# Optimization experiments

Measured on AMD Instinct MI355X. Metric: run time of the kernel, lower is better.

## Reference

```python
import jax, jax.numpy as jnp
import numpy as np

B, T, J = 8, 1024, 25
D_MODEL, D_STATE, D_CONV, EXPAND = 256, 16, 4, 2
D_INNER = EXPAND * D_MODEL            # 512
DT_RANK = (D_MODEL + 15) // 16        # 16
N_CLASSES = 60


def layernorm(x, g, b, eps=1e-5):
    mu = x.mean(-1, keepdims=True)
    var = ((x - mu) ** 2).mean(-1, keepdims=True)
    return (x - mu) * jax.lax.rsqrt(var + eps) * g + b


def selective_scan(u, delta, A, Bm, Cm, D):
    # u, delta: [b,l,d]; A: [d,n]; Bm, Cm: [b,l,n]; D: [d]
    dA = jnp.exp(delta[..., None] * A)                              # [b,l,d,n]
    dBu = delta[..., None] * Bm[:, :, None, :] * u[..., None]        # [b,l,d,n]

    def step(h, inp):
        dA_t, dBu_t, C_t = inp
        h = dA_t * h + dBu_t                                         # [b,d,n]
        y = jnp.einsum('bdn,bn->bd', h, C_t)
        return h, y

    h0 = jnp.zeros((u.shape[0], u.shape[2], A.shape[1]), u.dtype)
    _, ys = jax.lax.scan(step, h0, (jnp.moveaxis(dA, 1, 0),
                                    jnp.moveaxis(dBu, 1, 0),
                                    jnp.moveaxis(Cm, 1, 0)))
    return jnp.moveaxis(ys, 0, 1) + u * D                            # [b,l,d]


def setup_inputs() -> dict:
    key = jax.random.key(0)
    ks = jax.random.split(key, 12)
    rn = lambda k, s, sc=0.02: jax.random.normal(k, s, jnp.float32) * sc
    A_log = jnp.log(jnp.tile(jnp.arange(1, D_STATE + 1, dtype=jnp.float32), (D_INNER, 1)))
    return {
        'x': jax.random.normal(ks[0], (B, T, J, 3), jnp.float32),
        'embed_w': rn(ks[1], (D_MODEL, J * 9)), 'embed_b': jnp.zeros((D_MODEL,), jnp.float32),
        'pre_g': jnp.ones((D_MODEL,), jnp.float32), 'pre_b': jnp.zeros((D_MODEL,), jnp.float32),
        'in_proj_w': rn(ks[2], (2 * D_INNER, D_MODEL)),
        'conv_w': rn(ks[3], (D_INNER, 1, D_CONV)), 'conv_b': jnp.zeros((D_INNER,), jnp.float32),
        'x_proj_w': rn(ks[4], (DT_RANK + 2 * D_STATE, D_INNER)),
        'dt_proj_w': rn(ks[5], (D_INNER, DT_RANK)), 'dt_proj_b': rn(ks[6], (D_INNER,), 0.1),
        'A_log': A_log, 'D': jnp.ones((D_INNER,), jnp.float32),
        'out_proj_w': rn(ks[7], (D_MODEL, D_INNER)),
        'post_g': jnp.ones((D_MODEL,), jnp.float32), 'post_b': jnp.zeros((D_MODEL,), jnp.float32),
        'fine_w': rn(ks[8], (N_CLASSES, D_MODEL)), 'fine_b': jnp.zeros((N_CLASSES,), jnp.float32),
    }


def reference(x, embed_w, embed_b, pre_g, pre_b, in_proj_w, conv_w, conv_b,
              x_proj_w, dt_proj_w, dt_proj_b, A_log, D, out_proj_w,
              post_g, post_b, fine_w, fine_b):
    b, t = x.shape[0], x.shape[1]
    # --- SkeletonNormalizer: root-center (scale_joints=None) ---
    pos = x[..., :3] - x[:, :, 0:1, :3]                              # [B,T,J,3]
    # --- MotionFeatureBuilder: pos / vel / acc ---
    vel = jnp.concatenate([jnp.zeros_like(pos[:, :1]), pos[:, 1:] - pos[:, :-1]], axis=1)
    acc = jnp.concatenate([jnp.zeros_like(vel[:, :1]), vel[:, 1:] - vel[:, :-1]], axis=1)
    feat = jnp.concatenate([pos, vel, acc], axis=-1).reshape(b, t, -1)  # [B,T,J*9]
    # --- embed ---
    feat = feat @ embed_w.T + embed_b                                # [B,T,D_MODEL]
    # --- Mamba block on pre-norm, residual add ---
    hn = layernorm(feat, pre_g, pre_b)
    xz = hn @ in_proj_w.T                                            # [B,T,2*D_INNER]
    xm, res = jnp.split(xz, 2, axis=-1)
    # depthwise causal conv1d over time
    xm = jax.lax.conv_general_dilated(
        jnp.swapaxes(xm, 1, 2), conv_w, (1,), [(D_CONV - 1, 0)],
        dimension_numbers=('NCH', 'OIH', 'NCH'), feature_group_count=D_INNER)
    xm = jnp.swapaxes(xm + conv_b[None, :, None], 1, 2)              # [B,T,D_INNER]
    xm = jax.nn.silu(xm)
    dbl = xm @ x_proj_w.T                                            # [B,T,DT_RANK+2*D_STATE]
    dt = dbl[..., :DT_RANK]
    Bm = dbl[..., DT_RANK:DT_RANK + D_STATE]
    Cm = dbl[..., DT_RANK + D_STATE:]
    delta = jax.nn.softplus(dt @ dt_proj_w.T + dt_proj_b)            # [B,T,D_INNER]
    A = -jnp.exp(A_log)                                              # [D_INNER,D_STATE]
    y = selective_scan(xm, delta, A, Bm, Cm, D)
    y = y * jax.nn.silu(res)
    y = y @ out_proj_w.T                                             # [B,T,D_MODEL]
    feat = feat + y
    # --- post norm, mean pool, classify ---
    feat = layernorm(feat, post_g, post_b)
    pooled = feat.mean(axis=1)                                       # [B,D_MODEL]
    return pooled @ fine_w.T + fine_b                                # [B,N_CLASSES]
```

## Files before the change

kernel.cpp:

```cpp
#include <hip/hip_runtime.h>
#include <hip/hip_bf16.h>
#include <math.h>

#define Bb 8
#define Tt 1024
#define Jj 25
#define D_MODEL 256
#define D_STATE 16
#define D_CONV 4
#define D_INNER 512
#define DT_RANK 16
#define N_CLASSES 60
#define Mrows (Bb*Tt)
#define NC 64
#define CL 16

typedef unsigned short u16;
using bf16x8 = __attribute__((ext_vector_type(8))) __bf16;
using f32x4  = __attribute__((ext_vector_type(4))) float;

__device__ inline u16 f2bf(float x) {
    unsigned u = __float_as_uint(x);
    unsigned r = (u + 0x7fffu + ((u >> 16) & 1u)) >> 16;
    return (u16)r;
}
__device__ inline float bf2f(u16 h) { return __uint_as_float((unsigned)h << 16); }
__device__ inline void split2(float x, u16& h, u16& l) {
    h = f2bf(x);
    l = f2bf(x - bf2f(h));
}
__device__ inline float softplus_fast(float s) {
    return fmaxf(s, 0.f) + __logf(1.f + __expf(-fabsf(s)));
}
__device__ inline f32x4 mfma3(bf16x8 ah, bf16x8 al, bf16x8 bh, bf16x8 bl, f32x4 c) {
    c = __builtin_amdgcn_mfma_f32_16x16x32_bf16(al, bh, c, 0, 0, 0);
    c = __builtin_amdgcn_mfma_f32_16x16x32_bf16(ah, bl, c, 0, 0, 0);
    c = __builtin_amdgcn_mfma_f32_16x16x32_bf16(ah, bh, c, 0, 0, 0);
    return c;
}

__global__ __launch_bounds__(256) void prep_kernel(
    const float* __restrict__ x, u16* __restrict__ fh, u16* __restrict__ fl,
    const float* __restrict__ ew, const float* __restrict__ iw,
    const float* __restrict__ xw, const float* __restrict__ ow,
    u16* __restrict__ ebh, u16* __restrict__ ebl,
    u16* __restrict__ iph, u16* __restrict__ ipl,
    u16* __restrict__ xph, u16* __restrict__ xpl,
    u16* __restrict__ oph, u16* __restrict__ opl) {
    int blk = blockIdx.x;
    if (blk < Mrows) {
        int r = blk;
        int c = threadIdx.x;
        float v = 0.f;
        if (c < 225) {
            int t = r & (Tt - 1);
            int j = c / 9;
            int cc = c - j * 9;
            int comp = cc % 3;
            int kind = cc / 3;
            auto POS = [&](int dt) -> float {
                const float* p = x + (long)(r - dt) * Jj * 3;
                return p[j * 3 + comp] - p[comp];
            };
            if (kind == 0) v = POS(0);
            else if (kind == 1) v = (t >= 1) ? (POS(0) - POS(1)) : 0.f;
            else {
                if (t >= 2)      v = POS(0) - 2.f * POS(1) + POS(2);
                else if (t == 1) v = POS(0) - POS(1);
                else             v = 0.f;
            }
        }
        u16 h, l;
        split2(v, h, l);
        fh[(long)r * 256 + c] = h;
        fl[(long)r * 256 + c] = l;
    } else {
        int i = (blk - Mrows) * 256 + threadIdx.x;
        const float* src; u16 *dh, *dl; int K, kshift, idx;
        if (i < 65536)       { src = ew; dh = ebh; dl = ebl; K = 225; kshift = 8; idx = i; }
        else if (i < 327680) { src = iw; dh = iph; dl = ipl; K = 256; kshift = 8; idx = i - 65536; }
        else if (i < 352256) { src = xw; dh = xph; dl = xpl; K = 512; kshift = 9; idx = i - 327680; }
        else                 { src = ow; dh = oph; dl = opl; K = 512; kshift = 9; idx = i - 352256; }
        int n = idx >> kshift;
        int k = idx & ((1 << kshift) - 1);
        float v = (k < K) ? src[(long)n * K + k] : 0.f;
        u16 h, l;
        split2(v, h, l);
        dh[idx] = h;
        dl[idx] = l;
    }
}

template<int BM, int BN, int EPI>
__global__ __launch_bounds__(256) void gemm_mfma(
    const u16* __restrict__ Ahi, const u16* __restrict__ Alo, int lda,
    const u16* __restrict__ Whi, const u16* __restrict__ Wlo, int ldw,
    const float* __restrict__ bias, const float* __restrict__ resid, int ldr,
    float* __restrict__ C, int ldc, int M, int N, int K)
{
    constexpr int TM = BM / 32;
    constexpr int TN = BN / 32;
    constexpr int SA = 40;
    __shared__ u16 AsH[BM * SA], AsL[BM * SA];
    __shared__ u16 WsH[BN * SA], WsL[BN * SA];
    int tid = threadIdx.x;
    int m0 = blockIdx.y * BM;
    int n0 = blockIdx.x * BN;
    int lane = tid & 63;
    int wave = tid >> 6;
    int wm = wave >> 1, wn = wave & 1;
    int fr = lane & 15, quad = lane >> 4;
    f32x4 acc[TM][TN] = {};

    for (int k0 = 0; k0 < K; k0 += 32) {
        for (int s = tid; s < BM * 4; s += 256) {
            int row = s >> 2, seg = s & 3;
            long off = (long)(m0 + row) * lda + k0 + seg * 8;
            *(uint4*)&AsH[row * SA + seg * 8] = *(const uint4*)(Ahi + off);
            *(uint4*)&AsL[row * SA + seg * 8] = *(const uint4*)(Alo + off);
        }
        for (int s = tid; s < BN * 4; s += 256) {
            int row = s >> 2, seg = s & 3;
            long off = (long)(n0 + row) * ldw + k0 + seg * 8;
            *(uint4*)&WsH[row * SA + seg * 8] = *(const uint4*)(Whi + off);
            *(uint4*)&WsL[row * SA + seg * 8] = *(const uint4*)(Wlo + off);
        }
        __syncthreads();
        bf16x8 aH[TM], aL[TM], bH[TN], bL[TN];
#pragma unroll
        for (int im = 0; im < TM; im++) {
            int r = wm * (BM / 2) + im * 16 + fr;
            aH[im] = *(const bf16x8*)&AsH[r * SA + quad * 8];
            aL[im] = *(const bf16x8*)&AsL[r * SA + quad * 8];
        }
#pragma unroll
        for (int in = 0; in < TN; in++) {
            int r = wn * (BN / 2) + in * 16 + fr;
            bH[in] = *(const bf16x8*)&WsH[r * SA + quad * 8];
            bL[in] = *(const bf16x8*)&WsL[r * SA + quad * 8];
        }
#pragma unroll
        for (int im = 0; im < TM; im++)
#pragma unroll
            for (int in = 0; in < TN; in++)
                acc[im][in] = mfma3(aH[im], aL[im], bH[in], bL[in], acc[im][in]);
        __syncthreads();
    }
#pragma unroll
    for (int im = 0; im < TM; im++) {
#pragma unroll
        for (int in = 0; in < TN; in++) {
#pragma unroll
            for (int reg = 0; reg < 4; reg++) {
                int gm = m0 + wm * (BM / 2) + im * 16 + quad * 4 + reg;
                int gn = n0 + wn * (BN / 2) + in * 16 + fr;
                float v = acc[im][in][reg];
                if (EPI == 1) v += bias[gn];
                if (EPI == 3) v += resid[(long)gm * ldr + gn];
                C[(long)gm * ldc + gn] = v;
            }
        }
    }
}

__global__ __launch_bounds__(256) void ln_kernel(const float* __restrict__ x,
                                                 const float* __restrict__ g,
                                                 const float* __restrict__ b,
                                                 u16* outh, u16* outl) {
    __shared__ float red[256];
    long r = blockIdx.x;
    int d = threadIdx.x;
    float v = x[r * 256 + d];
    red[d] = v;
    __syncthreads();
    for (int s = 128; s > 0; s >>= 1) {
        if (d < s) red[d] += red[d + s];
        __syncthreads();
    }
    float mu = red[0] * (1.f / 256.f);
    __syncthreads();
    float dv = v - mu;
    red[d] = dv * dv;
    __syncthreads();
    for (int s = 128; s > 0; s >>= 1) {
        if (d < s) red[d] += red[d + s];
        __syncthreads();
    }
    float var = red[0] * (1.f / 256.f);
    float o = dv * rsqrtf(var + 1e-5f) * g[d] + b[d];
    u16 h, l;
    split2(o, h, l);
    outh[r * 256 + d] = h;
    outl[r * 256 + d] = l;
}

__global__ __launch_bounds__(256) void ln_pool_kernel(const float* __restrict__ x,
                                                      const float* __restrict__ g,
                                                      const float* __restrict__ b,
                                                      float* __restrict__ bp) {
    __shared__ float red[256];
    long r = blockIdx.x;
    int d = threadIdx.x;
    float v = x[r * 256 + d];
    red[d] = v;
    __syncthreads();
    for (int s = 128; s > 0; s >>= 1) {
        if (d < s) red[d] += red[d + s];
        __syncthreads();
    }
    float mu = red[0] * (1.f / 256.f);
    __syncthreads();
    float dv = v - mu;
    red[d] = dv * dv;
    __syncthreads();
    for (int s = 128; s > 0; s >>= 1) {
        if (d < s) red[d] += red[d + s];
        __syncthreads();
    }
    float var = red[0] * (1.f / 256.f);
    float o = dv * rsqrtf(var + 1e-5f) * g[d] + b[d];
    atomicAdd(&bp[(r >> 6) * 256 + d], o);
}

__global__ __launch_bounds__(256) void conv_xproj_kernel(
    const float* __restrict__ xz,
    const float* __restrict__ cw, const float* __restrict__ cb,
    const u16* __restrict__ Whi, const u16* __restrict__ Wlo,
    u16* __restrict__ xmh, u16* __restrict__ xml,
    float* __restrict__ dbl)
{
    constexpr int SA = 40;
    __shared__ u16 AsH[16 * SA], AsL[16 * SA];
    __shared__ u16 WsH[64 * SA], WsL[64 * SA];
    int tid = threadIdx.x;
    int m0 = blockIdx.x * 16;
    int lane = tid & 63, wave = tid >> 6;
    int fr = lane & 15, quad = lane >> 4;
    f32x4 acc = {};

    if (tid < 64) {
        int wr = 48 + (tid >> 2), seg = tid & 3;
        *(uint4*)&WsH[wr * SA + seg * 8] = make_uint4(0, 0, 0, 0);
        *(uint4*)&WsL[wr * SA + seg * 8] = make_uint4(0, 0, 0, 0);
    }

    int row = tid >> 4;
    int cg  = tid & 15;
    long gr = m0 + row;
    int t = gr & (Tt - 1);
    const float* xzr = xz + gr * 1024;

    for (int k0 = 0; k0 < 512; k0 += 32) {
        int c0 = k0 + cg * 2;
        float2 x0 = *(const float2*)(xzr + c0);
        float2 x1 = (t >= 1) ? *(const float2*)(xzr - 1024 + c0) : make_float2(0, 0);
        float2 x2 = (t >= 2) ? *(const float2*)(xzr - 2048 + c0) : make_float2(0, 0);
        float2 x3 = (t >= 3) ? *(const float2*)(xzr - 3072 + c0) : make_float2(0, 0);
        u16 hh0, ll0, hh1, ll1;
        {
            float4 w = *(const float4*)(cw + (c0 + 0) * 4);
            float a = cb[c0 + 0] + w.w * x0.x + w.z * x1.x + w.y * x2.x + w.x * x3.x;
            float s = a / (1.f + __expf(-a));
            split2(s, hh0, ll0);
            w = *(const float4*)(cw + (c0 + 1) * 4);
            a = cb[c0 + 1] + w.w * x0.y + w.z * x1.y + w.y * x2.y + w.x * x3.y;
            s = a / (1.f + __expf(-a));
            split2(s, hh1, ll1);
        }
        unsigned ph = hh0 | ((unsigned)hh1 << 16);
        unsigned pl = ll0 | ((unsigned)ll1 << 16);
        *(unsigned*)(xmh + gr * 512 + c0) = ph;
        *(unsigned*)(xml + gr * 512 + c0) = pl;
        *(unsigned*)&AsH[row * SA + cg * 2] = ph;
        *(unsigned*)&AsL[row * SA + cg * 2] = pl;
        if (tid < 192) {
            int wr = tid >> 2, seg = tid & 3;
            long off = (long)wr * 512 + k0 + seg * 8;
            *(uint4*)&WsH[wr * SA + seg * 8] = *(const uint4*)(Whi + off);
            *(uint4*)&WsL[wr * SA + seg * 8] = *(const uint4*)(Wlo + off);
        }
        __syncthreads();
        bf16x8 aH = *(const bf16x8*)&AsH[fr * SA + quad * 8];
        bf16x8 aL = *(const bf16x8*)&AsL[fr * SA + quad * 8];
        int wrow = wave * 16 + fr;
        bf16x8 bH = *(const bf16x8*)&WsH[wrow * SA + quad * 8];
        bf16x8 bL = *(const bf16x8*)&WsL[wrow * SA + quad * 8];
        acc = mfma3(aH, aL, bH, bL, acc);
        __syncthreads();
    }
    int gn = wave * 16 + fr;
    if (gn < 48) {
#pragma unroll
        for (int reg = 0; reg < 4; reg++) {
            int gm = m0 + quad * 4 + reg;
            dbl[(long)gm * 48 + gn] = acc[reg];
        }
    }
}

__global__ __launch_bounds__(512) void scan_p1(const float* __restrict__ dbl,
                                               const float* __restrict__ dtw,
                                               const float* __restrict__ dtb,
                                               const u16* __restrict__ xmh,
                                               const u16* __restrict__ xml,
                                               const float* __restrict__ A_log,
                                               float* __restrict__ chunkS,
                                               float* __restrict__ sumdelta) {
    __shared__ float ds[CL * 48];
    int b = blockIdx.x, c = blockIdx.y, d = threadIdx.x;
    long r0 = (long)b * Tt + (long)c * CL;
    for (int i = d; i < CL * 48; i += 512) ds[i] = dbl[r0 * 48 + i];

    float Arow[16];
#pragma unroll
    for (int n = 0; n < 16; n++) Arow[n] = -expf(A_log[d * 16 + n]);
    float4 wd[4];
#pragma unroll
    for (int q = 0; q < 4; q++) wd[q] = *(const float4*)(dtw + d * 16 + q * 4);
    float bdt = dtb[d];
    float S[16];
#pragma unroll
    for (int n = 0; n < 16; n++) S[n] = 0.f;
    float sd = 0.f;
    __syncthreads();

    for (int t = 0; t < CL; t++) {
        const float* row = ds + t * 48;
        float4 t0 = *(const float4*)(row + 0);
        float4 t1 = *(const float4*)(row + 4);
        float4 t2 = *(const float4*)(row + 8);
        float4 t3 = *(const float4*)(row + 12);
        float s = bdt;
        s += t0.x * wd[0].x + t0.y * wd[0].y + t0.z * wd[0].z + t0.w * wd[0].w;
        s += t1.x * wd[1].x + t1.y * wd[1].y + t1.z * wd[1].z + t1.w * wd[1].w;
        s += t2.x * wd[2].x + t2.y * wd[2].y + t2.z * wd[2].z + t2.w * wd[2].w;
        s += t3.x * wd[3].x + t3.y * wd[3].y + t3.z * wd[3].z + t3.w * wd[3].w;
        float dl = softplus_fast(s);
        long r = r0 + t;
        float u = bf2f(xmh[r * 512 + d]) + bf2f(xml[r * 512 + d]);
        float du = dl * u;
        sd += dl;
        float Bn[16];
#pragma unroll
        for (int q = 0; q < 4; q++) {
            float4 bv = *(const float4*)(row + 16 + q * 4);
            Bn[q*4+0] = bv.x; Bn[q*4+1] = bv.y; Bn[q*4+2] = bv.z; Bn[q*4+3] = bv.w;
        }
#pragma unroll
        for (int n = 0; n < 16; n++) {
            float a = __expf(dl * Arow[n]);
            S[n] = a * S[n] + du * Bn[n];
        }
    }
    long base = ((long)(b * NC + c) * 16) * 512 + d;
#pragma unroll
    for (int n = 0; n < 16; n++) chunkS[base + (long)n * 512] = S[n];
    sumdelta[(long)(b * NC + c) * 512 + d] = sd;
}

__global__ __launch_bounds__(256) void scan_combine(float* chunkS,
                                                    const float* __restrict__ sumdelta,
                                                    const float* __restrict__ A_log) {
    int idx = blockIdx.x * 256 + threadIdx.x;
    int d = idx & 511;
    int n = (idx >> 9) & 15;
    int b = idx >> 13;
    float Aval = -expf(A_log[d * 16 + n]);
    float h = 0.f;
    for (int c = 0; c < NC; c++) {
        long si = ((long)(b * NC + c) * 16 + n) * 512 + d;
        float s = chunkS[si];
        float a = __expf(Aval * sumdelta[(long)(b * NC + c) * 512 + d]);
        chunkS[si] = h;
        h = a * h + s;
    }
}

__global__ __launch_bounds__(512) void scan_p2(const float* __restrict__ dbl,
                                               const float* __restrict__ dtw,
                                               const float* __restrict__ dtb,
                                               const u16* xmh, const u16* xml,
                                               const float* __restrict__ xz,
                                               const float* __restrict__ A_log,
                                               const float* __restrict__ Dv,
                                               const float* __restrict__ chunkH,
                                               u16* yh, u16* yl) {
    __shared__ float ds[CL * 48];
    int b = blockIdx.x, c = blockIdx.y, d = threadIdx.x;
    long r0 = (long)b * Tt + (long)c * CL;
    for (int i = d; i < CL * 48; i += 512) ds[i] = dbl[r0 * 48 + i];

    float Arow[16];
#pragma unroll
    for (int n = 0; n < 16; n++) Arow[n] = -expf(A_log[d * 16 + n]);
    float4 wd[4];
#pragma unroll
    for (int q = 0; q < 4; q++) wd[q] = *(const float4*)(dtw + d * 16 + q * 4);
    float bdt = dtb[d];
    float Dd = Dv[d];
    float h[16];
    long base = ((long)(b * NC + c) * 16) * 512 + d;
#pragma unroll
    for (int n = 0; n < 16; n++) h[n] = chunkH[base + (long)n * 512];
    __syncthreads();

    for (int t = 0; t < CL; t++) {
        const float* row = ds + t * 48;
        float4 t0 = *(const float4*)(row + 0);
        float4 t1 = *(const float4*)(row + 4);
        float4 t2 = *(const float4*)(row + 8);
        float4 t3 = *(const float4*)(row + 12);
        float s = bdt;
        s += t0.x * wd[0].x + t0.y * wd[0].y + t0.z * wd[0].z + t0.w * wd[0].w;
        s += t1.x * wd[1].x + t1.y * wd[1].y + t1.z * wd[1].z + t1.w * wd[1].w;
        s += t2.x * wd[2].x + t2.y * wd[2].y + t2.z * wd[2].z + t2.w * wd[2].w;
        s += t3.x * wd[3].x + t3.y * wd[3].y + t3.z * wd[3].z + t3.w * wd[3].w;
        float dl = softplus_fast(s);
        long r = r0 + t;
        float u = bf2f(xmh[r * 512 + d]) + bf2f(xml[r * 512 + d]);
        float res = xz[r * 1024 + 512 + d];
        float du = dl * u;
        float Bn[16], Cn[16];
#pragma unroll
        for (int q = 0; q < 4; q++) {
            float4 bv = *(const float4*)(row + 16 + q * 4);
            float4 cv = *(const float4*)(row + 32 + q * 4);
            Bn[q*4+0] = bv.x; Bn[q*4+1] = bv.y; Bn[q*4+2] = bv.z; Bn[q*4+3] = bv.w;
            Cn[q*4+0] = cv.x; Cn[q*4+1] = cv.y; Cn[q*4+2] = cv.z; Cn[q*4+3] = cv.w;
        }
        float ysum = 0.f;
#pragma unroll
        for (int n = 0; n < 16; n++) {
            float a = __expf(dl * Arow[n]);
            h[n] = a * h[n] + du * Bn[n];
            ysum += h[n] * Cn[n];
        }
        float yy = ysum + u * Dd;
        float sres = res / (1.f + __expf(-res));
        float outv = yy * sres;
        u16 hh, ll;
        split2(outv, hh, ll);
        yh[r * 512 + d] = hh;
        yl[r * 512 + d] = ll;
    }
}

__global__ __launch_bounds__(256) void head_kernel(const float* __restrict__ bp,
                                                   const float* __restrict__ fw,
                                                   const float* __restrict__ fb,
                                                   float* __restrict__ out) {
    __shared__ float pld[256];
    int b = blockIdx.x;
    int d = threadIdx.x;
    float s = 0.f;
#pragma unroll
    for (int i = 0; i < 16; i++)
        s += bp[(long)(b * 16 + i) * 256 + d];
    pld[d] = s;
    __syncthreads();
    if (d < N_CLASSES) {
        float acc = 0.f;
        for (int k = 0; k < 256; k++) acc += pld[k] * fw[d * 256 + k];
        out[b * N_CLASSES + d] = acc * (1.f / (float)Tt) + fb[d];
    }
}

extern "C" void kernel_launch(void* const* d_in, const int* in_sizes, int n_in,
                              void* d_out, int out_size, void* d_ws, size_t ws_size,
                              hipStream_t stream) {
    const float* x         = (const float*)d_in[0];
    const float* embed_w   = (const float*)d_in[1];
    const float* embed_b   = (const float*)d_in[2];
    const float* pre_g     = (const float*)d_in[3];
    const float* pre_b     = (const float*)d_in[4];
    const float* in_proj_w = (const float*)d_in[5];
    const float* conv_w    = (const float*)d_in[6];
    const float* conv_b    = (const float*)d_in[7];
    const float* x_proj_w  = (const float*)d_in[8];
    const float* dt_proj_w = (const float*)d_in[9];
    const float* dt_proj_b = (const float*)d_in[10];
    const float* A_log     = (const float*)d_in[11];
    const float* Dv        = (const float*)d_in[12];
    const float* out_proj_w= (const float*)d_in[13];
    const float* post_g    = (const float*)d_in[14];
    const float* post_b    = (const float*)d_in[15];
    const float* fine_w    = (const float*)d_in[16];
    const float* fine_b    = (const float*)d_in[17];
    float* out = (float*)d_out;
    char* base = (char*)d_ws;

    float* feat     = (float*)(base + 0);
    float* xz       = (float*)(base + 8388608);
    float* chunkS   = (float*)(base + 41943040);
    u16*   xmh      = (u16*)  (base + 58720256);
    u16*   xml      = (u16*)  (base + 67108864);
    u16*   fbh      = (u16*)  (base + 75497472);
    u16*   fbl      = (u16*)  (base + 79691776);
    float* dbl      = (float*)(base + 83886080);
    float* sumdelta = (float*)(base + 85458944);
    float* blockpart= (float*)(base + 86507520);
    u16*   ebh      = (u16*)  (base + 86638592);
    u16*   ebl      = ebh + 65536;
    u16*   iph      = ebl + 65536;
    u16*   ipl      = iph + 262144;
    u16*   xph      = ipl + 262144;
    u16*   xpl      = xph + 24576;
    u16*   oph      = xpl + 24576;
    u16*   opl      = oph + 131072;

    prep_kernel<<<dim3(Mrows + 1888), dim3(256), 0, stream>>>(
        x, fbh, fbl, embed_w, in_proj_w, x_proj_w, out_proj_w,
        ebh, ebl, iph, ipl, xph, xpl, oph, opl);

    gemm_mfma<64,64,1><<<dim3(4, 128), dim3(256), 0, stream>>>(
        fbh, fbl, 256, ebh, ebl, 256, embed_b, nullptr, 0, feat, 256, Mrows, 256, 256);

    ln_kernel<<<dim3(Mrows), dim3(256), 0, stream>>>(feat, pre_g, pre_b, fbh, fbl);

    gemm_mfma<128,64,0><<<dim3(16, 64), dim3(256), 0, stream>>>(
        fbh, fbl, 256, iph, ipl, 256, nullptr, nullptr, 0, xz, 1024, Mrows, 1024, 256);

    conv_xproj_kernel<<<dim3(Mrows / 16), dim3(256), 0, stream>>>(
        xz, conv_w, conv_b, xph, xpl, xmh, xml, dbl);

    scan_p1<<<dim3(Bb, NC), dim3(512), 0, stream>>>(
        dbl, dt_proj_w, dt_proj_b, xmh, xml, A_log, chunkS, sumdelta);
    scan_combine<<<dim3(256), dim3(256), 0, stream>>>(chunkS, sumdelta, A_log);
    scan_p2<<<dim3(Bb, NC), dim3(512), 0, stream>>>(
        dbl, dt_proj_w, dt_proj_b, xmh, xml, xz, A_log, Dv, chunkS, xmh, xml);

    gemm_mfma<64,64,3><<<dim3(4, 128), dim3(256), 0, stream>>>(
        xmh, xml, 512, oph, opl, 512, nullptr, feat, 256, feat, 256, Mrows, 256, 512);

    hipMemsetAsync(blockpart, 0, 128 * 256 * sizeof(float), stream);
    ln_pool_kernel<<<dim3(Mrows), dim3(256), 0, stream>>>(feat, post_g, post_b, blockpart);

    head_kernel<<<dim3(Bb), dim3(256), 0, stream>>>(blockpart, fine_w, fine_b, out);
}
```

Measured before the change: 260.9 us.

## Fuse chunked scan phases into one cooperative kernel with grid syncs

Merges scan_p1, scan_combine and scan_p2 into a single cooperative kernel separated by grid.sync. Each block keeps its chunk's dt-projection inputs, A row and u values in registers across phases, so the second pass no longer reloads xm or recomputes setup. The blockpart memset moves into extra blocks of the prep kernel, and the loops are reshaped to read B and C directly from float4. This trades two launches for grid-wide barriers, adds register pressure from uu[16], and leaves most blocks idle during the combine phase.

```diff
diff --git a/kernel.cpp b/kernel.cpp
--- a/kernel.cpp
+++ b/kernel.cpp
@@ -1,6 +1,9 @@
 #include <hip/hip_runtime.h>
 #include <hip/hip_bf16.h>
+#include <hip/hip_cooperative_groups.h>
 #include <math.h>
+
+namespace cg = cooperative_groups;
 
 #define Bb 8
 #define Tt 1024
@@ -46,7 +49,8 @@
     u16* __restrict__ ebh, u16* __restrict__ ebl,
     u16* __restrict__ iph, u16* __restrict__ ipl,
     u16* __restrict__ xph, u16* __restrict__ xpl,
-    u16* __restrict__ oph, u16* __restrict__ opl) {
+    u16* __restrict__ oph, u16* __restrict__ opl,
+    float* __restrict__ blockpart) {
     int blk = blockIdx.x;
     if (blk < Mrows) {
         int r = blk;
@@ -74,7 +78,7 @@
         split2(v, h, l);
         fh[(long)r * 256 + c] = h;
         fl[(long)r * 256 + c] = l;
-    } else {
+    } else if (blk < Mrows + 1888) {
         int i = (blk - Mrows) * 256 + threadIdx.x;
         const float* src; u16 *dh, *dl; int K, kshift, idx;
         if (i < 65536)       { src = ew; dh = ebh; dl = ebl; K = 225; kshift = 8; idx = i; }
@@ -88,6 +92,9 @@
         split2(v, h, l);
         dh[idx] = h;
         dl[idx] = l;
+    } else {
+        int i = (blk - Mrows - 1888) * 256 + threadIdx.x;
+        blockpart[i] = 0.f;
     }
 }
 
@@ -298,14 +305,16 @@
     }
 }
 
-__global__ __launch_bounds__(512) void scan_p1(const float* __restrict__ dbl,
-                                               const float* __restrict__ dtw,
-                                               const float* __restrict__ dtb,
-                                               const u16* __restrict__ xmh,
-                                               const u16* __restrict__ xml,
-                                               const float* __restrict__ A_log,
-                                               float* __restrict__ chunkS,
-                                               float* __restrict__ sumdelta) {
+__global__ __launch_bounds__(512, 4) void scan_fused(
+    const float* __restrict__ dbl,
+    const float* __restrict__ dtw, const float* __restrict__ dtb,
+    const u16* xmh, const u16* xml,
+    const float* __restrict__ xz,
+    const float* __restrict__ A_log, const float* __restrict__ Dv,
+    float* chunkS, float* sumdelta,
+    u16* yh, u16* yl)
+{
+    cg::grid_group grid = cg::this_grid();
     __shared__ float ds[CL * 48];
     int b = blockIdx.x, c = blockIdx.y, d = threadIdx.x;
     long r0 = (long)b * Tt + (long)c * CL;
@@ -318,6 +327,7 @@
 #pragma unroll
     for (int q = 0; q < 4; q++) wd[q] = *(const float4*)(dtw + d * 16 + q * 4);
     float bdt = dtb[d];
+    float uu[CL];
     float S[16];
 #pragma unroll
     for (int n = 0; n < 16; n++) S[n] = 0.f;
@@ -338,71 +348,50 @@
         float dl = softplus_fast(s);
         long r = r0 + t;
         float u = bf2f(xmh[r * 512 + d]) + bf2f(xml[r * 512 + d]);
+        uu[t] = u;
         float du = dl * u;
         sd += dl;
-        float Bn[16];
 #pragma unroll
         for (int q = 0; q < 4; q++) {
             float4 bv = *(const float4*)(row + 16 + q * 4);
-            Bn[q*4+0] = bv.x; Bn[q*4+1] = bv.y; Bn[q*4+2] = bv.z; Bn[q*4+3] = bv.w;
-        }
-#pragma unroll
-        for (int n = 0; n < 16; n++) {
-            float a = __expf(dl * Arow[n]);
-            S[n] = a * S[n] + du * Bn[n];
-        }
-    }
-    long base = ((long)(b * NC + c) * 16) * 512 + d;
-#pragma unroll
-    for (int n = 0; n < 16; n++) chunkS[base + (long)n * 512] = S[n];
+            float a0 = __expf(dl * Arow[q*4+0]); S[q*4+0] = a0 * S[q*4+0] + du * bv.x;
+            float a1 = __expf(dl * Arow[q*4+1]); S[q*4+1] = a1 * S[q*4+1] + du * bv.y;
+            float a2 = __expf(dl * Arow[q*4+2]); S[q*4+2] = a2 * S[q*4+2] + du * bv.z;
+            float a3 = __expf(dl * Arow[q*4+3]); S[q*4+3] = a3 * S[q*4+3] + du * bv.w;
+        }
+    }
+    long basei = ((long)(b * NC + c) * 16) * 512 + d;
+#pragma unroll
+    for (int n = 0; n < 16; n++) chunkS[basei + (long)n * 512] = S[n];
     sumdelta[(long)(b * NC + c) * 512 + d] = sd;
-}
-
-__global__ __launch_bounds__(256) void scan_combine(float* chunkS,
-                                                    const float* __restrict__ sumdelta,
-                                                    const float* __restrict__ A_log) {
-    int idx = blockIdx.x * 256 + threadIdx.x;
-    int d = idx & 511;
-    int n = (idx >> 9) & 15;
-    int b = idx >> 13;
-    float Aval = -expf(A_log[d * 16 + n]);
-    float h = 0.f;
-    for (int c = 0; c < NC; c++) {
-        long si = ((long)(b * NC + c) * 16 + n) * 512 + d;
-        float s = chunkS[si];
-        float a = __expf(Aval * sumdelta[(long)(b * NC + c) * 512 + d]);
-        chunkS[si] = h;
-        h = a * h + s;
-    }
-}
-
-__global__ __launch_bounds__(512) void scan_p2(const float* __restrict__ dbl,
-                                               const float* __restrict__ dtw,
-                                               const float* __restrict__ dtb,
-                                               const u16* xmh, const u16* xml,
-                                               const float* __restrict__ xz,
-                                               const float* __restrict__ A_log,
-                                               const float* __restrict__ Dv,
-                                               const float* __restrict__ chunkH,
-                                               u16* yh, u16* yl) {
-    __shared__ float ds[CL * 48];
-    int b = blockIdx.x, c = blockIdx.y, d = threadIdx.x;
-    long r0 = (long)b * Tt + (long)c * CL;
-    for (int i = d; i < CL * 48; i += 512) ds[i] = dbl[r0 * 48 + i];
-
-    float Arow[16];
-#pragma unroll
-    for (int n = 0; n < 16; n++) Arow[n] = -expf(A_log[d * 16 + n]);
-    float4 wd[4];
-#pragma unroll
-    for (int q = 0; q < 4; q++) wd[q] = *(const float4*)(dtw + d * 16 + q * 4);
-    float bdt = dtb[d];
+
+    __threadfence();
+    grid.sync();
+
+    int bid = blockIdx.y * 8 + blockIdx.x;
+    if (bid < 128) {
+        int idx = bid * 512 + d;
+        int dd = idx & 511;
+        int nn = (idx >> 9) & 15;
+        int bb = idx >> 13;
+        float Aval = -expf(A_log[dd * 16 + nn]);
+        float h = 0.f;
+        for (int cc = 0; cc < NC; cc++) {
+            long si = ((long)(bb * NC + cc) * 16 + nn) * 512 + dd;
+            float s = chunkS[si];
+            float a = __expf(Aval * sumdelta[(long)(bb * NC + cc) * 512 + dd]);
+            chunkS[si] = h;
+            h = a * h + s;
+        }
+    }
+
+    __threadfence();
+    grid.sync();
+
     float Dd = Dv[d];
     float h[16];
-    long base = ((long)(b * NC + c) * 16) * 512 + d;
-#pragma unroll
-    for (int n = 0; n < 16; n++) h[n] = chunkH[base + (long)n * 512];
-    __syncthreads();
+#pragma unroll
+    for (int n = 0; n < 16; n++) h[n] = chunkS[basei + (long)n * 512];
 
     for (int t = 0; t < CL; t++) {
         const float* row = ds + t * 48;
@@ -417,23 +406,18 @@
         s += t3.x * wd[3].x + t3.y * wd[3].y + t3.z * wd[3].z + t3.w * wd[3].w;
         float dl = softplus_fast(s);
         long r = r0 + t;
-        float u = bf2f(xmh[r * 512 + d]) + bf2f(xml[r * 512 + d]);
+        float u = uu[t];
         float res = xz[r * 1024 + 512 + d];
         float du = dl * u;
-        float Bn[16], Cn[16];
+        float ysum = 0.f;
 #pragma unroll
         for (int q = 0; q < 4; q++) {
             float4 bv = *(const float4*)(row + 16 + q * 4);
             float4 cv = *(const float4*)(row + 32 + q * 4);
-            Bn[q*4+0] = bv.x; Bn[q*4+1] = bv.y; Bn[q*4+2] = bv.z; Bn[q*4+3] = bv.w;
-            Cn[q*4+0] = cv.x; Cn[q*4+1] = cv.y; Cn[q*4+2] = cv.z; Cn[q*4+3] = cv.w;
-        }
-        float ysum = 0.f;
-#pragma unroll
-        for (int n = 0; n < 16; n++) {
-            float a = __expf(dl * Arow[n]);
-            h[n] = a * h[n] + du * Bn[n];
-            ysum += h[n] * Cn[n];
+            float a0 = __expf(dl * Arow[q*4+0]); h[q*4+0] = a0 * h[q*4+0] + du * bv.x; ysum += h[q*4+0] * cv.x;
+            float a1 = __expf(dl * Arow[q*4+1]); h[q*4+1] = a1 * h[q*4+1] + du * bv.y; ysum += h[q*4+1] * cv.y;
+            float a2 = __expf(dl * Arow[q*4+2]); h[q*4+2] = a2 * h[q*4+2] + du * bv.z; ysum += h[q*4+2] * cv.z;
+            float a3 = __expf(dl * Arow[q*4+3]); h[q*4+3] = a3 * h[q*4+3] + du * bv.w; ysum += h[q*4+3] * cv.w;
         }
         float yy = ysum + u * Dd;
         float sres = res / (1.f + __expf(-res));
@@ -508,9 +492,9 @@
     u16*   oph      = xpl + 24576;
     u16*   opl      = oph + 131072;
 
-    prep_kernel<<<dim3(Mrows + 1888), dim3(256), 0, stream>>>(
+    prep_kernel<<<dim3(Mrows + 1888 + 128), dim3(256), 0, stream>>>(
         x, fbh, fbl, embed_w, in_proj_w, x_proj_w, out_proj_w,
-        ebh, ebl, iph, ipl, xph, xpl, oph, opl);
+        ebh, ebl, iph, ipl, xph, xpl, oph, opl, blockpart);
 
     gemm_mfma<64,64,1><<<dim3(4, 128), dim3(256), 0, stream>>>(
         fbh, fbl, 256, ebh, ebl, 256, embed_b, nullptr, 0, feat, 256, Mrows, 256, 256);
@@ -523,16 +507,21 @@
     conv_xproj_kernel<<<dim3(Mrows / 16), dim3(256), 0, stream>>>(
         xz, conv_w, conv_b, xph, xpl, xmh, xml, dbl);
 
-    scan_p1<<<dim3(Bb, NC), dim3(512), 0, stream>>>(
-        dbl, dt_proj_w, dt_proj_b, xmh, xml, A_log, chunkS, sumdelta);
-    scan_combine<<<dim3(256), dim3(256), 0, stream>>>(chunkS, sumdelta, A_log);
-    scan_p2<<<dim3(Bb, NC), dim3(512), 0, stream>>>(
-        dbl, dt_proj_w, dt_proj_b, xmh, xml, xz, A_log, Dv, chunkS, xmh, xml);
+    {
+        void* args[] = {
+            (void*)&dbl, (void*)&dt_proj_w, (void*)&dt_proj_b,
+            (void*)&xmh, (void*)&xml, (void*)&xz,
+            (void*)&A_log, (void*)&Dv,
+            (void*)&chunkS, (void*)&sumdelta,
+            (void*)&xmh, (void*)&xml
+        };
+        hipLaunchCooperativeKernel((void*)scan_fused, dim3(Bb, NC), dim3(512),
+                                   args, 0, stream);
+    }
 
     gemm_mfma<64,64,3><<<dim3(4, 128), dim3(256), 0, stream>>>(
         xmh, xml, 512, oph, opl, 512, nullptr, feat, 256, feat, 256, Mrows, 256, 512);
 
-    hipMemsetAsync(blockpart, 0, 128 * 256 * sizeof(float), stream);
     ln_pool_kernel<<<dim3(Mrows), dim3(256), 0, stream>>>(feat, post_g, post_b, blockpart);
 
     head_kernel<<<dim3(Bb), dim3(256), 0, stream>>>(blockpart, fine_w, fine_b, out);
```

Result: slower. 596.8 us (+128.8%).
